# Kernel tuning notes

Hardware: AMD Instinct MI355X
Metric: run time of the kernel (lower is better)

## Reference

```python
import jax, jax.numpy as jnp
import numpy as np

N, K, D = 65536, 1024, 256
COMMIT = 0.25
EPS = 1e-12


def setup_inputs() -> dict:
    key = jax.random.key(0)
    kx, kw = jax.random.split(key)
    x = jax.random.normal(kx, (N, D), dtype=jnp.float32)
    # nn.Embedding weight init: uniform(-1/vector_num, 1/vector_num)
    weight = jax.random.uniform(kw, (K, D), dtype=jnp.float32,
                                minval=-1.0 / K, maxval=1.0 / K)
    return {"x": x, "weight": weight}


def reference(x, weight):
    distances = (jnp.sum(x * x, axis=1, keepdims=True)
                 + jnp.sum(weight * weight, axis=1)
                 - 2.0 * (x @ weight.T))
    vector_indices = jnp.argmin(distances, axis=1)              # [N]
    quantized = weight[vector_indices]                          # gather == one-hot @ weight

    e_latent_loss = jnp.mean((jax.lax.stop_gradient(quantized) - x) ** 2)
    q_latent_loss = jnp.mean((quantized - jax.lax.stop_gradient(x)) ** 2)
    quant_loss = q_latent_loss + COMMIT * e_latent_loss

    # straight-through estimator
    quantized_out = x + jax.lax.stop_gradient(quantized - x)

    # utilization: counts of each code (== column sums of one-hot encodings)
    counts = jnp.zeros((K,), x.dtype).at[vector_indices].add(1.0)
    util_loss = jnp.mean(jnp.abs(counts - x.shape[0] / K))

    # compactness: 2 * mean of pairwise euclidean distances among codebook rows
    sq = jnp.sum(weight * weight, axis=1)
    pd2 = sq[:, None] + sq[None, :] - 2.0 * (weight @ weight.T)  # [K, K]
    iu = jnp.triu(jnp.ones((K, K), bool), 1)
    pd = jnp.sqrt(jnp.maximum(jnp.where(iu, pd2, 1.0), EPS))
    n_pairs = K * (K - 1) // 2
    compact_loss = 2.0 * jnp.sum(jnp.where(iu, pd, 0.0)) / n_pairs

    return quantized_out, quant_loss, util_loss, compact_loss, vector_indices
```

## Files before the change

kernel.cpp:

```cpp
#include <hip/hip_runtime.h>
#include <math.h>

#define NROWS 65536
#define KCODES 1024
#define DDIM 256
#define ND_TOT (NROWS * DDIM)

#define WS_IDX      0
#define WS_COUNTS   262144
#define WS_SW       266240
#define WS_PARTQ    532480
#define WS_PARTP    536576
#define WS_FLAGCNT  540672
#define WS_FLAGLIST 540928
#define WS_WH       803072
#define WS_WL       1327360

typedef float f32x4 __attribute__((ext_vector_type(4)));
typedef short bf16x8 __attribute__((ext_vector_type(8)));

__device__ inline unsigned short f2bf(float f) {
  unsigned u = __float_as_uint(f);
  u += 0x7FFFu + ((u >> 16) & 1u);
  return (unsigned short)(u >> 16);
}
__device__ inline float bf2f(unsigned short h) {
  return __uint_as_float(((unsigned)h) << 16);
}

__device__ inline void gload16(const void* g, void* l) {
  __builtin_amdgcn_global_load_lds((const __attribute__((address_space(1))) void*)g,
                                   (__attribute__((address_space(3))) void*)l, 16, 0, 0);
}

__global__ __launch_bounds__(256) void vq_prep(const float* __restrict__ x,
                                               const float* __restrict__ w,
                                               unsigned short* __restrict__ xh,
                                               unsigned short* __restrict__ xl,
                                               float* __restrict__ sw,
                                               unsigned short* __restrict__ wh,
                                               unsigned short* __restrict__ wl,
                                               int* __restrict__ counts,
                                               int* __restrict__ flagCnt,
                                               float* __restrict__ partialP) {
#pragma clang fp contract(off)
  const int b = blockIdx.x;
  const int t = threadIdx.x;
  if (b >= 2048) {
    const int lane = t & 63, wv = t >> 6;
    const int row = (b - 2048) * 4 + wv;
    const float* src = w + (size_t)row * DDIM;
    float4 v4 = *(const float4*)&src[lane * 4];
    float fv[4] = {v4.x, v4.y, v4.z, v4.w};
    union { unsigned short us[4]; uint2 v; } ph, pl;
#pragma unroll
    for (int e = 0; e < 4; ++e) {
      unsigned short h = f2bf(fv[e]);
      ph.us[e] = h;
      pl.us[e] = f2bf(fv[e] - bf2f(h));
    }
    *(uint2*)&wh[(size_t)row * DDIM + lane * 4] = ph.v;
    *(uint2*)&wl[(size_t)row * DDIM + lane * 4] = pl.v;
    float acc = 0.f;
    if (lane < 16) {
      const float* p = src + ((lane >> 3) & 1) * 128 + (lane & 7);
      float v = p[0];
      acc = v * v;
      for (int k = 1; k < 16; ++k) { float vv = p[k * 8]; float e = vv * vv; acc = acc + e; }
    }
    acc = acc + __shfl_xor(acc, 1);
    acc = acc + __shfl_xor(acc, 2);
    acc = acc + __shfl_xor(acc, 4);
    const float hb = __shfl(acc, 8);
    if (lane == 0) sw[row] = acc + hb;
    return;
  }
  if (b == 0) {
#pragma unroll
    for (int j = 0; j < 4; ++j) { counts[j * 256 + t] = 0; partialP[j * 256 + t] = 0.f; }
    if (t == 0) flagCnt[0] = 0;
  }
  const size_t tid = (size_t)b * 256 + t;
  float4 a[4], c[4];
#pragma unroll
  for (int g = 0; g < 4; ++g) {
    const size_t e = ((size_t)g * 524288 + tid) * 8;
    a[g] = *(const float4*)&x[e];
    c[g] = *(const float4*)&x[e + 4];
  }
#pragma unroll
  for (int g = 0; g < 4; ++g) {
    const size_t e = ((size_t)g * 524288 + tid) * 8;
    float fv[8] = {a[g].x, a[g].y, a[g].z, a[g].w, c[g].x, c[g].y, c[g].z, c[g].w};
    union { unsigned short us[8]; uint4 v; } ph, pl;
#pragma unroll
    for (int k = 0; k < 8; ++k) {
      unsigned short h = f2bf(fv[k]);
      ph.us[k] = h;
      pl.us[k] = f2bf(fv[k] - bf2f(h));
    }
    *(uint4*)&xh[e] = ph.v;
    *(uint4*)&xl[e] = pl.v;
  }
}

#define TRM 128
#define BKM 64
#define REPAIR_T 1.5e-4f

__global__ __launch_bounds__(256, 2) void vq_argmin_mfma(
    const unsigned short* __restrict__ xh, const unsigned short* __restrict__ xl,
    const unsigned short* __restrict__ wh, const unsigned short* __restrict__ wl,
    const float* __restrict__ sw,
    int* __restrict__ idxOut, float* __restrict__ idxOutF,
    int* __restrict__ flagCnt, int* __restrict__ flagList) {
  __shared__ __align__(16) unsigned short lds_wh[TRM * BKM];
  __shared__ __align__(16) unsigned short lds_wl[TRM * BKM];
  __shared__ __align__(16) float sws[KCODES];
  __shared__ float mrgB1[TRM];
  __shared__ float mrgB2[TRM];
  __shared__ int   mrgI[TRM];

  const int t = threadIdx.x;
  const int lane = t & 63, wv = t >> 6;
  const int row0 = blockIdx.x * TRM;

  { f32x4 v = ((const f32x4*)sw)[t]; ((f32x4*)sws)[t] = v; }

  const int laneRow = lane >> 3;
  const int srcswz = ((lane & 7) * 16) ^ ((laneRow & 7) << 4);
  const char* whB = (const char*)wh;
  const char* wlB = (const char*)wl;

  bf16x8 ah[2][8], al[2][8];
  {
    const int rbase = row0 + wv * 32 + (lane & 15);
    const int kof = ((lane >> 4) & 3) * 8;
#pragma unroll
    for (int i = 0; i < 2; ++i)
#pragma unroll
      for (int ks = 0; ks < 8; ++ks) {
        const size_t e = (size_t)(rbase + i * 16) * DDIM + (size_t)(ks * 32 + kof);
        ah[i][ks] = *(const bf16x8*)&xh[e];
        al[i][ks] = *(const bf16x8*)&xl[e];
      }
  }

  float b1[8], b2[8];
  int bi[8];
#pragma unroll
  for (int s = 0; s < 8; ++s) { b1[s] = 3.4e38f; b2[s] = 3.4e38f; bi[s] = 0; }

  for (int ct = 0; ct < KCODES / TRM; ++ct) {
    f32x4 acc[2][8];
#pragma unroll
    for (int i = 0; i < 2; ++i)
#pragma unroll
      for (int j = 0; j < 8; ++j) acc[i][j] = (f32x4){0.f, 0.f, 0.f, 0.f};

    for (int dt = 0; dt < 4; ++dt) {
      __syncthreads();
#pragma unroll
      for (int i = 0; i < 4; ++i) {
        const int rb = wv * 32 + i * 8;
        const size_t gow = (size_t)(ct * 128 + rb + laneRow) * 512 + (size_t)(dt * 128 + srcswz);
        gload16(whB + gow, (char*)lds_wh + rb * 128);
        gload16(wlB + gow, (char*)lds_wl + rb * 128);
      }
      __syncthreads();

#pragma unroll
      for (int kh = 0; kh < 2; ++kh) {
        const int kb = kh * 64 + ((lane >> 4) & 3) * 16;
        const int ks = dt * 2 + kh;
#pragma unroll
        for (int j = 0; j < 8; ++j) {
          const int c = j * 16 + (lane & 15);
          const int off = c * 128 + (kb ^ ((c & 7) << 4));
          bf16x8 bh = *(const bf16x8*)((const char*)lds_wh + off);
          bf16x8 bl = *(const bf16x8*)((const char*)lds_wl + off);
#pragma unroll
          for (int i = 0; i < 2; ++i) {
            acc[i][j] = __builtin_amdgcn_mfma_f32_16x16x32_bf16(ah[i][ks], bh, acc[i][j], 0, 0, 0);
            acc[i][j] = __builtin_amdgcn_mfma_f32_16x16x32_bf16(ah[i][ks], bl, acc[i][j], 0, 0, 0);
            acc[i][j] = __builtin_amdgcn_mfma_f32_16x16x32_bf16(al[i][ks], bh, acc[i][j], 0, 0, 0);
          }
        }
      }
    }

#pragma unroll
    for (int j = 0; j < 8; ++j) {
      const int colbase = ct * 128 + j * 16 + (lane & 15);
      const float swv = sws[colbase];
#pragma unroll
      for (int i = 0; i < 2; ++i)
#pragma unroll
        for (int q = 0; q < 4; ++q) {
          const int s = i * 4 + q;
          const float e = fmaf(-2.f, acc[i][j][q], swv);
          const bool c1 = e < b1[s];
          b2[s] = c1 ? b1[s] : fminf(b2[s], e);
          bi[s] = c1 ? colbase : bi[s];
          b1[s] = fminf(b1[s], e);
        }
    }
  }

#pragma unroll
  for (int off = 1; off < 16; off <<= 1) {
#pragma unroll
    for (int s = 0; s < 8; ++s) {
      const float ob1 = __shfl_xor(b1[s], off);
      const float ob2 = __shfl_xor(b2[s], off);
      const int oi = __shfl_xor(bi[s], off);
      const float hi = fmaxf(b1[s], ob1);
      const bool take = ob1 < b1[s];
      b1[s] = fminf(b1[s], ob1);
      b2[s] = fminf(hi, fminf(b2[s], ob2));
      bi[s] = take ? oi : bi[s];
    }
  }
  if ((lane & 15) == 0) {
#pragma unroll
    for (int i = 0; i < 2; ++i)
#pragma unroll
      for (int q = 0; q < 4; ++q) {
        const int s = i * 4 + q;
        const int r = wv * 32 + i * 16 + ((lane >> 4) & 3) * 4 + q;
        mrgB1[r] = b1[s]; mrgB2[r] = b2[s]; mrgI[r] = bi[s];
      }
  }
  __syncthreads();
  if (t < TRM) {
    const float b1f = mrgB1[t];
    const float b2f = mrgB2[t];
    const int idxf = mrgI[t];
    const int grow = row0 + t;
    idxOut[grow] = idxf;
    idxOutF[grow] = (float)idxf;
    const bool flag = (b2f - b1f) < REPAIR_T;
    unsigned long long m = __ballot(flag);
    int base2 = 0;
    if ((t & 63) == 0) base2 = atomicAdd(flagCnt, __popcll(m));
    base2 = __shfl(base2, 0);
    if (flag) flagList[base2 + __popcll(m & ((1ull << (t & 63)) - 1ull))] = grow;
  }
}

#define RPB 8
__global__ __launch_bounds__(256) void vq_repair(
    const float* __restrict__ x, const float* __restrict__ w,
    const float* __restrict__ sw,
    const int* __restrict__ flagCnt, const int* __restrict__ flagList,
    int* __restrict__ idxOut, float* __restrict__ idxOutF) {
  const int t = threadIdx.x;
  const int lane = t & 63, wvid = t >> 6;
  __shared__ __align__(16) float xrow[RPB][DDIM];
  __shared__ float sxsh[RPB];
  __shared__ float redD[RPB][4];
  __shared__ int   redI[RPB][4];
  const int cnt = flagCnt[0];
  for (int base = blockIdx.x * RPB; base < cnt; base += 1024 * RPB) {
    const int nr = min(RPB, cnt - base);
    __syncthreads();
    for (int r = 0; r < nr; ++r)
      xrow[r][t] = x[(size_t)flagList[base + r] * DDIM + t];
    __syncthreads();
    if (t < nr) {
#pragma clang fp contract(off)
      float halves[2];
#pragma unroll
      for (int h = 0; h < 2; ++h) {
        const float* p = &xrow[t][h * 128];
        float acc[8];
#pragma unroll
        for (int j = 0; j < 8; ++j) { float v = p[j]; acc[j] = v * v; }
        for (int i = 8; i < 128; i += 8) {
#pragma unroll
          for (int j = 0; j < 8; ++j) { float v = p[i + j]; float e = v * v; acc[j] = acc[j] + e; }
        }
        halves[h] = ((acc[0] + acc[1]) + (acc[2] + acc[3])) + ((acc[4] + acc[5]) + (acc[6] + acc[7]));
      }
      sxsh[t] = halves[0] + halves[1];
    }
    __syncthreads();
    float acc[4][RPB];
#pragma unroll
    for (int g = 0; g < 4; ++g)
#pragma unroll
      for (int r = 0; r < RPB; ++r) acc[g][r] = 0.f;
    const float4* wrp0 = (const float4*)(w + (size_t)(0 * 256 + t) * DDIM);
    const float4* wrp1 = (const float4*)(w + (size_t)(1 * 256 + t) * DDIM);
    const float4* wrp2 = (const float4*)(w + (size_t)(2 * 256 + t) * DDIM);
    const float4* wrp3 = (const float4*)(w + (size_t)(3 * 256 + t) * DDIM);
    for (int d4 = 0; d4 < DDIM / 4; ++d4) {
      float4 xr4[RPB];
#pragma unroll
      for (int r = 0; r < RPB; ++r) xr4[r] = *(const float4*)&xrow[r][d4 * 4];
      const float4 wv0 = wrp0[d4], wv1 = wrp1[d4], wv2 = wrp2[d4], wv3 = wrp3[d4];
#pragma unroll
      for (int e = 0; e < 4; ++e) {
        const float w0 = (e == 0) ? wv0.x : (e == 1) ? wv0.y : (e == 2) ? wv0.z : wv0.w;
        const float w1 = (e == 0) ? wv1.x : (e == 1) ? wv1.y : (e == 2) ? wv1.z : wv1.w;
        const float w2 = (e == 0) ? wv2.x : (e == 1) ? wv2.y : (e == 2) ? wv2.z : wv2.w;
        const float w3 = (e == 0) ? wv3.x : (e == 1) ? wv3.y : (e == 2) ? wv3.z : wv3.w;
#pragma unroll
        for (int r = 0; r < RPB; ++r) {
          const float xv = (e == 0) ? xr4[r].x : (e == 1) ? xr4[r].y : (e == 2) ? xr4[r].z : xr4[r].w;
          acc[0][r] = fmaf(xv, w0, acc[0][r]);
          acc[1][r] = fmaf(xv, w1, acc[1][r]);
          acc[2][r] = fmaf(xv, w2, acc[2][r]);
          acc[3][r] = fmaf(xv, w3, acc[3][r]);
        }
      }
    }
    float bD[RPB]; int bI[RPB];
#pragma unroll
    for (int r = 0; r < RPB; ++r) { bD[r] = 3.4e38f; bI[r] = 0x7fffffff; }
#pragma unroll
    for (int g = 0; g < 4; ++g) {
      const int c = g * 256 + t;
      const float swc = sw[c];
#pragma unroll
      for (int r = 0; r < RPB; ++r) {
        const float tt = sxsh[r] + swc;
        const float dist = tt - 2.0f * acc[g][r];
        if (dist < bD[r]) { bD[r] = dist; bI[r] = c; }
      }
    }
#pragma unroll
    for (int off = 32; off > 0; off >>= 1) {
#pragma unroll
      for (int r = 0; r < RPB; ++r) {
        const float od = __shfl_down(bD[r], off);
        const int oi = __shfl_down(bI[r], off);
        if (od < bD[r] || (od == bD[r] && oi < bI[r])) { bD[r] = od; bI[r] = oi; }
      }
    }
    if (lane == 0) {
#pragma unroll
      for (int r = 0; r < RPB; ++r) { redD[r][wvid] = bD[r]; redI[r][wvid] = bI[r]; }
    }
    __syncthreads();
    if (t < nr) {
      float bb = redD[t][0]; int bix = redI[t][0];
#pragma unroll
      for (int k = 1; k < 4; ++k) {
        const float od = redD[t][k]; const int oi = redI[t][k];
        if (od < bb || (od == bb && oi < bix)) { bb = od; bix = oi; }
      }
      const int row = flagList[base + t];
      idxOut[row] = bix;
      idxOutF[row] = (float)bix;
    }
  }
}

#define CTI 32
#define CPAD 260
__global__ __launch_bounds__(256) void vq_compact(const float* __restrict__ w,
                                                  const float* __restrict__ sw,
                                                  float* __restrict__ partialP) {
  __shared__ __align__(16) float wI[CTI][CPAD];
  __shared__ __align__(16) float wJ[CTI][CPAD];
  const int t = threadIdx.x;
  const int lane = t & 63, wvid = t >> 6;
  int b = blockIdx.x, ti = 0;
  while (b >= 32 - ti) { b -= 32 - ti; ++ti; }
  const int tj = ti + b;
#pragma unroll
  for (int k = 0; k < 8; ++k) {
    const int q = k * 256 + t;
    const int r = q >> 6, c4 = q & 63;
    float4 vI = *(const float4*)&w[(size_t)(ti * CTI + r) * DDIM + c4 * 4];
    float4 vJ = *(const float4*)&w[(size_t)(tj * CTI + r) * DDIM + c4 * 4];
    *(float4*)&wI[r][c4 * 4] = vI;
    *(float4*)&wJ[r][c4 * 4] = vJ;
  }
  __syncthreads();
  const int ia = 2 * (t & 15);
  const int jc = 2 * (t >> 4);
  float a00 = 0.f, a01 = 0.f, a10 = 0.f, a11 = 0.f;
  for (int d4 = 0; d4 < DDIM / 4; ++d4) {
    const float4 A0 = *(const float4*)&wI[ia][d4 * 4];
    const float4 A1 = *(const float4*)&wI[ia + 1][d4 * 4];
    const float4 B0 = *(const float4*)&wJ[jc][d4 * 4];
    const float4 B1 = *(const float4*)&wJ[jc + 1][d4 * 4];
    a00 += A0.x * B0.x + A0.y * B0.y + A0.z * B0.z + A0.w * B0.w;
    a01 += A0.x * B1.x + A0.y * B1.y + A0.z * B1.z + A0.w * B1.w;
    a10 += A1.x * B0.x + A1.y * B0.y + A1.z * B0.z + A1.w * B0.w;
    a11 += A1.x * B1.x + A1.y * B1.y + A1.z * B1.z + A1.w * B1.w;
  }
  double s = 0.0;
  {
    const int i0 = ti * CTI + ia, j0 = tj * CTI + jc;
    const float acc2[2][2] = {{a00, a01}, {a10, a11}};
#pragma unroll
    for (int ii = 0; ii < 2; ++ii)
#pragma unroll
      for (int jj = 0; jj < 2; ++jj) {
        const int i = i0 + ii, j = j0 + jj;
        if (i < j) {
          const float pd2 = (sw[i] + sw[j]) - 2.0f * acc2[ii][jj];
          s += (double)sqrtf(fmaxf(pd2, 1e-12f));
        }
      }
  }
  for (int off = 32; off > 0; off >>= 1) s += __shfl_down(s, off);
  __shared__ double redc[4];
  if (lane == 0) redc[wvid] = s;
  __syncthreads();
  if (t == 0) partialP[blockIdx.x] = (float)(redc[0] + redc[1] + redc[2] + redc[3]);
}

__global__ __launch_bounds__(256) void vq_quantize(const float* __restrict__ x,
                                                   const float* __restrict__ w,
                                                   const int* __restrict__ idxArr,
                                                   float* __restrict__ qout,
                                                   int* __restrict__ counts,
                                                   float* __restrict__ partialQ) {
  const int wave = threadIdx.x >> 6;
  const int lane = threadIdx.x & 63;
  const int base = blockIdx.x * 64 + wave * 16;
  float s = 0.f;
#pragma unroll
  for (int rg = 0; rg < 4; ++rg) {
    int idx4[4];
#pragma unroll
    for (int r = 0; r < 4; ++r) idx4[r] = idxArr[base + rg * 4 + r];
    float4 xv[4], qv[4];
#pragma unroll
    for (int r = 0; r < 4; ++r) {
      xv[r] = ((const float4*)(x + (size_t)(base + rg * 4 + r) * DDIM))[lane];
      qv[r] = ((const float4*)(w + (size_t)idx4[r] * DDIM))[lane];
    }
#pragma unroll
    for (int r = 0; r < 4; ++r) {
      const int row = base + rg * 4 + r;
      float dx = qv[r].x - xv[r].x, dy = qv[r].y - xv[r].y;
      float dz = qv[r].z - xv[r].z, dw = qv[r].w - xv[r].w;
      float4 o;
      o.x = xv[r].x + dx; o.y = xv[r].y + dy; o.z = xv[r].z + dz; o.w = xv[r].w + dw;
      ((float4*)(qout + (size_t)row * DDIM))[lane] = o;
      s += dx * dx + dy * dy + dz * dz + dw * dw;
      if (lane == 0) atomicAdd(&counts[idx4[r]], 1);
    }
  }
  double d = s;
  for (int off = 32; off > 0; off >>= 1) d += __shfl_down(d, off);
  __shared__ double red[4];
  if (lane == 0) red[wave] = d;
  __syncthreads();
  if (threadIdx.x == 0)
    partialQ[blockIdx.x] = (float)(red[0] + red[1] + red[2] + red[3]);
}

__global__ __launch_bounds__(1024) void vq_final(const float* __restrict__ partialQ,
                                                 const float* __restrict__ partialP,
                                                 const int* __restrict__ counts,
                                                 float* __restrict__ out) {
  const int t = threadIdx.x;
  const int lane = t & 63, wave = t >> 6;
  double q = (double)partialQ[t];
  double p = (double)partialP[t];
  double u = (double)fabsf((float)counts[t] - 64.0f);
  for (int off = 32; off > 0; off >>= 1) {
    q += __shfl_down(q, off);
    p += __shfl_down(p, off);
    u += __shfl_down(u, off);
  }
  __shared__ double redQ[16], redP[16], redU[16];
  if (lane == 0) { redQ[wave] = q; redP[wave] = p; redU[wave] = u; }
  __syncthreads();
  if (t == 0) {
    double sq = 0, sp = 0, su = 0;
    for (int j = 0; j < 16; ++j) { sq += redQ[j]; sp += redP[j]; su += redU[j]; }
    float m = (float)(sq / 16777216.0);
    out[ND_TOT] = m + 0.25f * m;
    out[ND_TOT + 1] = (float)(su / 1024.0);
    out[ND_TOT + 2] = (float)(2.0 * sp / 523776.0);
  }
}

extern "C" void kernel_launch(void* const* d_in, const int* in_sizes, int n_in,
                              void* d_out, int out_size, void* d_ws, size_t ws_size,
                              hipStream_t stream) {
  const float* x = (const float*)d_in[0];
  const float* w = (const float*)d_in[1];
  float* out = (float*)d_out;

  char* ws = (char*)d_ws;
  int* wsIdx    = (int*)(ws + WS_IDX);
  int* counts   = (int*)(ws + WS_COUNTS);
  float* swv    = (float*)(ws + WS_SW);
  float* partQ  = (float*)(ws + WS_PARTQ);
  float* partP  = (float*)(ws + WS_PARTP);
  int* flagCnt  = (int*)(ws + WS_FLAGCNT);
  int* flagList = (int*)(ws + WS_FLAGLIST);
  unsigned short* whS = (unsigned short*)(ws + WS_WH);
  unsigned short* wlS = (unsigned short*)(ws + WS_WL);

  unsigned short* xhS = (unsigned short*)d_out;
  unsigned short* xlS = xhS + (size_t)ND_TOT;

  vq_prep<<<2304, 256, 0, stream>>>(x, w, xhS, xlS, swv, whS, wlS, counts, flagCnt, partP);
  vq_argmin_mfma<<<NROWS / TRM, 256, 0, stream>>>(xhS, xlS, whS, wlS, swv,
                                                  wsIdx, out + ND_TOT + 3, flagCnt, flagList);
  vq_repair<<<1024, 256, 0, stream>>>(x, w, swv, flagCnt, flagList, wsIdx, out + ND_TOT + 3);
  vq_compact<<<528, 256, 0, stream>>>(w, swv, partP);
  vq_quantize<<<1024, 256, 0, stream>>>(x, w, wsIdx, out, counts, partQ);
  vq_final<<<1, 1024, 0, stream>>>(partQ, partP, counts, out);
}
```

Baseline: 236.6 us.

## Double-buffer codebook LDS tiles in argmin and merge repair with compact kernel

The argmin MFMA kernel now keeps two LDS buffers for the codebook tiles and issues the global-to-LDS loads for the next tile before computing on the current one, so the main loop has one barrier instead of two. The repair and compactness kernels are combined into one launch, with block ranges picking which role a block plays, which saves a launch and lets the two independent workloads run side by side. Double buffering doubles the codebook LDS footprint and may lower occupancy. The merged kernel's LDS use is set by the larger compact branch, which could limit residency for the repair blocks.

```diff
diff --git a/kernel.cpp b/kernel.cpp
--- a/kernel.cpp
+++ b/kernel.cpp
@@ -114,8 +114,8 @@
     const float* __restrict__ sw,
     int* __restrict__ idxOut, float* __restrict__ idxOutF,
     int* __restrict__ flagCnt, int* __restrict__ flagList) {
-  __shared__ __align__(16) unsigned short lds_wh[TRM * BKM];
-  __shared__ __align__(16) unsigned short lds_wl[TRM * BKM];
+  __shared__ __align__(16) unsigned short lds_wh[2][TRM * BKM];
+  __shared__ __align__(16) unsigned short lds_wl[2][TRM * BKM];
   __shared__ __align__(16) float sws[KCODES];
   __shared__ float mrgB1[TRM];
   __shared__ float mrgB2[TRM];
@@ -132,6 +132,18 @@
   const char* whB = (const char*)wh;
   const char* wlB = (const char*)wl;
 
+#define STAGE_W(CT, DT, BUF)                                                          \
+  {                                                                                   \
+    _Pragma("unroll")                                                                 \
+    for (int i_ = 0; i_ < 4; ++i_) {                                                  \
+      const int rb_ = wv * 32 + i_ * 8;                                               \
+      const size_t gow_ = (size_t)((CT) * 128 + rb_ + laneRow) * 512 +                \
+                          (size_t)((DT) * 128 + srcswz);                              \
+      gload16(whB + gow_, (char*)lds_wh[BUF] + rb_ * 128);                            \
+      gload16(wlB + gow_, (char*)lds_wl[BUF] + rb_ * 128);                            \
+    }                                                                                 \
+  }
+
   bf16x8 ah[2][8], al[2][8];
   {
     const int rbase = row0 + wv * 32 + (lane & 15);
@@ -151,6 +163,10 @@
 #pragma unroll
   for (int s = 0; s < 8; ++s) { b1[s] = 3.4e38f; b2[s] = 3.4e38f; bi[s] = 0; }
 
+  STAGE_W(0, 0, 0);
+  __syncthreads();
+  int cur = 0;
+
   for (int ct = 0; ct < KCODES / TRM; ++ct) {
     f32x4 acc[2][8];
 #pragma unroll
@@ -159,15 +175,9 @@
       for (int j = 0; j < 8; ++j) acc[i][j] = (f32x4){0.f, 0.f, 0.f, 0.f};
 
     for (int dt = 0; dt < 4; ++dt) {
-      __syncthreads();
-#pragma unroll
-      for (int i = 0; i < 4; ++i) {
-        const int rb = wv * 32 + i * 8;
-        const size_t gow = (size_t)(ct * 128 + rb + laneRow) * 512 + (size_t)(dt * 128 + srcswz);
-        gload16(whB + gow, (char*)lds_wh + rb * 128);
-        gload16(wlB + gow, (char*)lds_wl + rb * 128);
-      }
-      __syncthreads();
+      const int nct = (dt == 3) ? ct + 1 : ct;
+      const int ndt = (dt == 3) ? 0 : dt + 1;
+      if (nct < KCODES / TRM) STAGE_W(nct, ndt, cur ^ 1);
 
 #pragma unroll
       for (int kh = 0; kh < 2; ++kh) {
@@ -177,8 +187,8 @@
         for (int j = 0; j < 8; ++j) {
           const int c = j * 16 + (lane & 15);
           const int off = c * 128 + (kb ^ ((c & 7) << 4));
-          bf16x8 bh = *(const bf16x8*)((const char*)lds_wh + off);
-          bf16x8 bl = *(const bf16x8*)((const char*)lds_wl + off);
+          bf16x8 bh = *(const bf16x8*)((const char*)lds_wh[cur] + off);
+          bf16x8 bl = *(const bf16x8*)((const char*)lds_wl[cur] + off);
 #pragma unroll
           for (int i = 0; i < 2; ++i) {
             acc[i][j] = __builtin_amdgcn_mfma_f32_16x16x32_bf16(ah[i][ks], bh, acc[i][j], 0, 0, 0);
@@ -187,6 +197,8 @@
           }
         }
       }
+      __syncthreads();
+      cur ^= 1;
     }
 
 #pragma unroll
@@ -246,16 +258,71 @@
     base2 = __shfl(base2, 0);
     if (flag) flagList[base2 + __popcll(m & ((1ull << (t & 63)) - 1ull))] = grow;
   }
+#undef STAGE_W
 }
 
 #define RPB 8
-__global__ __launch_bounds__(256) void vq_repair(
+#define CTI 32
+#define CPAD 260
+__global__ __launch_bounds__(256) void vq_repair_compact(
     const float* __restrict__ x, const float* __restrict__ w,
     const float* __restrict__ sw,
     const int* __restrict__ flagCnt, const int* __restrict__ flagList,
-    int* __restrict__ idxOut, float* __restrict__ idxOutF) {
+    int* __restrict__ idxOut, float* __restrict__ idxOutF,
+    float* __restrict__ partialP) {
   const int t = threadIdx.x;
   const int lane = t & 63, wvid = t >> 6;
+  if (blockIdx.x >= 1024) {
+    __shared__ __align__(16) float wI[CTI][CPAD];
+    __shared__ __align__(16) float wJ[CTI][CPAD];
+    int b = blockIdx.x - 1024, ti = 0;
+    while (b >= 32 - ti) { b -= 32 - ti; ++ti; }
+    const int tj = ti + b;
+#pragma unroll
+    for (int k = 0; k < 8; ++k) {
+      const int q = k * 256 + t;
+      const int r = q >> 6, c4 = q & 63;
+      float4 vI = *(const float4*)&w[(size_t)(ti * CTI + r) * DDIM + c4 * 4];
+      float4 vJ = *(const float4*)&w[(size_t)(tj * CTI + r) * DDIM + c4 * 4];
+      *(float4*)&wI[r][c4 * 4] = vI;
+      *(float4*)&wJ[r][c4 * 4] = vJ;
+    }
+    __syncthreads();
+    const int ia = 2 * (t & 15);
+    const int jc = 2 * (t >> 4);
+    float a00 = 0.f, a01 = 0.f, a10 = 0.f, a11 = 0.f;
+    for (int d4 = 0; d4 < DDIM / 4; ++d4) {
+      const float4 A0 = *(const float4*)&wI[ia][d4 * 4];
+      const float4 A1 = *(const float4*)&wI[ia + 1][d4 * 4];
+      const float4 B0 = *(const float4*)&wJ[jc][d4 * 4];
+      const float4 B1 = *(const float4*)&wJ[jc + 1][d4 * 4];
+      a00 += A0.x * B0.x + A0.y * B0.y + A0.z * B0.z + A0.w * B0.w;
+      a01 += A0.x * B1.x + A0.y * B1.y + A0.z * B1.z + A0.w * B1.w;
+      a10 += A1.x * B0.x + A1.y * B0.y + A1.z * B0.z + A1.w * B0.w;
+      a11 += A1.x * B1.x + A1.y * B1.y + A1.z * B1.z + A1.w * B1.w;
+    }
+    double s = 0.0;
+    {
+      const int i0 = ti * CTI + ia, j0 = tj * CTI + jc;
+      const float acc2[2][2] = {{a00, a01}, {a10, a11}};
+#pragma unroll
+      for (int ii = 0; ii < 2; ++ii)
+#pragma unroll
+        for (int jj = 0; jj < 2; ++jj) {
+          const int i = i0 + ii, j = j0 + jj;
+          if (i < j) {
+            const float pd2 = (sw[i] + sw[j]) - 2.0f * acc2[ii][jj];
+            s += (double)sqrtf(fmaxf(pd2, 1e-12f));
+          }
+        }
+    }
+    for (int off = 32; off > 0; off >>= 1) s += __shfl_down(s, off);
+    __shared__ double redc[4];
+    if (lane == 0) redc[wvid] = s;
+    __syncthreads();
+    if (t == 0) partialP[blockIdx.x - 1024] = (float)(redc[0] + redc[1] + redc[2] + redc[3]);
+    return;
+  }
   __shared__ __align__(16) float xrow[RPB][DDIM];
   __shared__ float sxsh[RPB];
   __shared__ float redD[RPB][4];
@@ -357,63 +424,6 @@
   }
 }
 
-#define CTI 32
-#define CPAD 260
-__global__ __launch_bounds__(256) void vq_compact(const float* __restrict__ w,
-                                                  const float* __restrict__ sw,
-                                                  float* __restrict__ partialP) {
-  __shared__ __align__(16) float wI[CTI][CPAD];
-  __shared__ __align__(16) float wJ[CTI][CPAD];
-  const int t = threadIdx.x;
-  const int lane = t & 63, wvid = t >> 6;
-  int b = blockIdx.x, ti = 0;
-  while (b >= 32 - ti) { b -= 32 - ti; ++ti; }
-  const int tj = ti + b;
-#pragma unroll
-  for (int k = 0; k < 8; ++k) {
-    const int q = k * 256 + t;
-    const int r = q >> 6, c4 = q & 63;
-    float4 vI = *(const float4*)&w[(size_t)(ti * CTI + r) * DDIM + c4 * 4];
-    float4 vJ = *(const float4*)&w[(size_t)(tj * CTI + r) * DDIM + c4 * 4];
-    *(float4*)&wI[r][c4 * 4] = vI;
-    *(float4*)&wJ[r][c4 * 4] = vJ;
-  }
-  __syncthreads();
-  const int ia = 2 * (t & 15);
-  const int jc = 2 * (t >> 4);
-  float a00 = 0.f, a01 = 0.f, a10 = 0.f, a11 = 0.f;
-  for (int d4 = 0; d4 < DDIM / 4; ++d4) {
-    const float4 A0 = *(const float4*)&wI[ia][d4 * 4];
-    const float4 A1 = *(const float4*)&wI[ia + 1][d4 * 4];
-    const float4 B0 = *(const float4*)&wJ[jc][d4 * 4];
-    const float4 B1 = *(const float4*)&wJ[jc + 1][d4 * 4];
-    a00 += A0.x * B0.x + A0.y * B0.y + A0.z * B0.z + A0.w * B0.w;
-    a01 += A0.x * B1.x + A0.y * B1.y + A0.z * B1.z + A0.w * B1.w;
-    a10 += A1.x * B0.x + A1.y * B0.y + A1.z * B0.z + A1.w * B0.w;
-    a11 += A1.x * B1.x + A1.y * B1.y + A1.z * B1.z + A1.w * B1.w;
-  }
-  double s = 0.0;
-  {
-    const int i0 = ti * CTI + ia, j0 = tj * CTI + jc;
-    const float acc2[2][2] = {{a00, a01}, {a10, a11}};
-#pragma unroll
-    for (int ii = 0; ii < 2; ++ii)
-#pragma unroll
-      for (int jj = 0; jj < 2; ++jj) {
-        const int i = i0 + ii, j = j0 + jj;
-        if (i < j) {
-          const float pd2 = (sw[i] + sw[j]) - 2.0f * acc2[ii][jj];
-          s += (double)sqrtf(fmaxf(pd2, 1e-12f));
-        }
-      }
-  }
-  for (int off = 32; off > 0; off >>= 1) s += __shfl_down(s, off);
-  __shared__ double redc[4];
-  if (lane == 0) redc[wvid] = s;
-  __syncthreads();
-  if (t == 0) partialP[blockIdx.x] = (float)(redc[0] + redc[1] + redc[2] + redc[3]);
-}
-
 __global__ __launch_bounds__(256) void vq_quantize(const float* __restrict__ x,
                                                    const float* __restrict__ w,
                                                    const int* __restrict__ idxArr,
@@ -507,8 +517,8 @@
   vq_prep<<<2304, 256, 0, stream>>>(x, w, xhS, xlS, swv, whS, wlS, counts, flagCnt, partP);
   vq_argmin_mfma<<<NROWS / TRM, 256, 0, stream>>>(xhS, xlS, whS, wlS, swv,
                                                   wsIdx, out + ND_TOT + 3, flagCnt, flagList);
-  vq_repair<<<1024, 256, 0, stream>>>(x, w, swv, flagCnt, flagList, wsIdx, out + ND_TOT + 3);
-  vq_compact<<<528, 256, 0, stream>>>(w, swv, partP);
+  vq_repair_compact<<<1552, 256, 0, stream>>>(x, w, swv, flagCnt, flagList,
+                                              wsIdx, out + ND_TOT + 3, partP);
   vq_quantize<<<1024, 256, 0, stream>>>(x, w, wsIdx, out, counts, partQ);
   vq_final<<<1, 1024, 0, stream>>>(partQ, partP, counts, out);
 }
```

Result: slower. 265.1 us (+12.0%).
